# Kernel optimization log

Measured on AMD Instinct MI355X. Metric: run time of the kernel, lower is better.

## Reference

```python
import jax, jax.numpy as jnp
import numpy as np

B, T, C = 4, 4096, 1024
NEG_INF = -1e38


def setup_inputs() -> dict:
    key = jax.random.key(0)
    ks = jax.random.split(key, 5)
    scale = 0.02  # realistic init scale for CxC projections
    x = jax.random.normal(ks[0], (B, T, C), dtype=jnp.float32)
    key_w = jax.random.normal(ks[1], (C, C), dtype=jnp.float32) * scale
    value_w = jax.random.normal(ks[2], (C, C), dtype=jnp.float32) * scale
    receptance_w = jax.random.normal(ks[3], (C, C), dtype=jnp.float32) * scale
    output_w = jax.random.normal(ks[4], (C, C), dtype=jnp.float32) * scale
    # deterministic param init matching the module's __init__
    time_decay = -5.0 + 8.0 * (jnp.arange(C, dtype=jnp.float32) / (C - 1)) ** 0.7
    time_first = jnp.full((C,), -3.0, dtype=jnp.float32)
    # initial WKV state as in forward() when state is None
    aa0 = jnp.zeros((B, C), dtype=jnp.float32)
    bb0 = jnp.zeros((B, C), dtype=jnp.float32)
    pp0 = jnp.full((B, C), NEG_INF, dtype=jnp.float32)
    return dict(x=x, key_w=key_w, value_w=value_w, receptance_w=receptance_w,
                output_w=output_w, time_decay=time_decay, time_first=time_first,
                aa0=aa0, bb0=bb0, pp0=pp0)


def reference(x, key_w, value_w, receptance_w, output_w,
              time_decay, time_first, aa0, bb0, pp0):
    # projections (torch Linear: y = x @ W.T)
    k = jnp.einsum('btc,dc->btd', x, key_w)        # [B,T,C]
    v = jnp.einsum('btc,dc->btd', x, value_w)      # [B,T,C]
    r = jax.nn.sigmoid(jnp.einsum('btc,dc->btd', x, receptance_w))
    w = jnp.exp(time_decay)  # [C]
    u = time_first           # [C]

    def step(carry, kv):
        aa, bb, pp = carry           # each [B,C]
        kt, vt = kv                  # each [B,C]
        # output at this step (numerically stabilized exp weighting)
        ww = u + kt
        p = jnp.maximum(pp, ww)
        e1 = jnp.exp(pp - p)
        e2 = jnp.exp(ww - p)
        wkv = (e1 * aa + e2 * vt) / (e1 * bb + e2)
        # state update
        ww2 = pp - w
        p2 = jnp.maximum(ww2, kt)
        e1b = jnp.exp(ww2 - p2)
        e2b = jnp.exp(kt - p2)
        return (e1b * aa + e2b * vt, e1b * bb + e2b, p2), wkv

    k_t = jnp.swapaxes(k, 0, 1)  # [T,B,C]
    v_t = jnp.swapaxes(v, 0, 1)
    (aa, bb, pp), wkv = jax.lax.scan(step, (aa0, bb0, pp0), (k_t, v_t))
    wkv = jnp.swapaxes(wkv, 0, 1)  # [B,T,C]

    out = jnp.einsum('btc,dc->btd', r * wkv, output_w)
    return out, aa, bb, pp
```

## Files before the change

kernel.cpp:

```cpp
#include <hip/hip_runtime.h>
#include <stdint.h>

#define BDIM 4
#define TDIM 4096
#define CDIM 1024
#define MDIM (BDIM * TDIM)
#define SSEG 64
#define LSEG 64
#define NCH  (BDIM * CDIM)

#define GK   1024
#define GK2  2048
#define NT32 32

typedef __attribute__((ext_vector_type(8))) short bf16x8;
typedef __attribute__((ext_vector_type(4))) float f32x4;

__device__ __forceinline__ unsigned short f2bf(float f) {
    unsigned u = __builtin_bit_cast(unsigned, f);
    u = u + 0x7fffu + ((u >> 16) & 1u);
    return (unsigned short)(u >> 16);
}
__device__ __forceinline__ float bf2f(unsigned short h) {
    unsigned u = ((unsigned)h) << 16;
    return __builtin_bit_cast(float, u);
}

typedef __attribute__((address_space(1))) const unsigned int g_u32;
typedef __attribute__((address_space(3))) unsigned int l_u32;
__device__ __forceinline__ void gload_lds16(const void* g, void* l) {
    __builtin_amdgcn_global_load_lds((g_u32*)g, (l_u32*)l, 16, 0, 0);
}

__global__ void castall(const float* __restrict__ x,
                        const float* __restrict__ kw, const float* __restrict__ vw,
                        const float* __restrict__ rw, const float* __restrict__ ow,
                        unsigned short* __restrict__ xb,
                        unsigned short* __restrict__ wf, unsigned short* __restrict__ owb) {
    int i = blockIdx.x * 256 + threadIdx.x;
    const float* s;
    unsigned short* d;
    int j;
    if (i < 4194304) {
        s = x; d = xb; j = i;
    } else {
        int k = i - 4194304;
        int m = k >> 18; j = k & 262143;
        s = (m == 0) ? kw : (m == 1) ? vw : (m == 2) ? rw : ow;
        d = (m < 3) ? (wf + (size_t)m * 1048576) : owb;
    }
    float4 f = ((const float4*)s)[j];
    ushort4 o;
    o.x = f2bf(f.x); o.y = f2bf(f.y); o.z = f2bf(f.z); o.w = f2bf(f.w);
    ((ushort4*)d)[j] = o;
}


#define MFMA16(ACCROW, AREG, BREG)                                          \
    _Pragma("unroll") for (int a_ = 0; a_ < 4; ++a_)                        \
    _Pragma("unroll") for (int b_ = 0; b_ < 4; ++b_)                        \
        acc[ACCROW + a_][b_] = __builtin_amdgcn_mfma_f32_16x16x32_bf16(     \
            AREG[a_], BREG[b_], acc[ACCROW + a_][b_], 0, 0, 0);

#define KT32(T, BU, BN)                                                     \
  {                                                                         \
    const int slot  = (T) & 3;                                              \
    const int slotN = ((T) + 1) & 3;                                        \
                          \
    {                                                                       \
        const char* ab = shA + slot * 16384 + wm * 8192 + aoffc;            \
        _Pragma("unroll") for (int m_ = 0; m_ < 4; ++m_)                    \
            a47[m_] = *(const bf16x8*)(ab + (4 + m_) * 1024);               \
    }                                                                       \
    stage((T) + 3, 0);                                                      \
    __builtin_amdgcn_s_barrier();                                           \
    __builtin_amdgcn_s_setprio(1);                                          \
    MFMA16(0, a03, BU)                                                      \
    __builtin_amdgcn_s_setprio(0);                                          \
    if ((T) <= 28)      asm volatile("s_waitcnt vmcnt(6)" ::: "memory");    \
    else if ((T) == 29) asm volatile("s_waitcnt vmcnt(4)" ::: "memory");    \
    else if ((T) == 30) asm volatile("s_waitcnt vmcnt(0)" ::: "memory");    \
    __builtin_amdgcn_s_barrier();                                           \
                \
    if ((T) + 1 < NT32) {                                                   \
        const char* abN = shA + slotN * 16384 + wm * 8192 + aoffc;          \
        const char* bbN = shB + slotN * 16384 + wn * 4096 + aoffc;          \
        _Pragma("unroll") for (int m_ = 0; m_ < 4; ++m_)                    \
            a03[m_] = *(const bf16x8*)(abN + m_ * 1024);                    \
        _Pragma("unroll") for (int n_ = 0; n_ < 4; ++n_)                    \
            BN[n_] = *(const bf16x8*)(bbN + n_ * 1024);                     \
    }                                                                       \
    stage((T) + 3, 1);                                                      \
    __builtin_amdgcn_s_barrier();                                           \
    __builtin_amdgcn_s_setprio(1);                                          \
    MFMA16(4, a47, BU)                                                      \
    __builtin_amdgcn_s_setprio(0);                                          \
    __builtin_amdgcn_s_barrier();                                           \
  }

template <int MODE, int NT>
__global__ __launch_bounds__(512, 2) void gemm256(
    const unsigned short* __restrict__ A,
    const unsigned short* __restrict__ Bw,
    unsigned short* __restrict__ oK, unsigned short* __restrict__ oV,
    unsigned short* __restrict__ oR, float* __restrict__ oF)
{
    extern __shared__ char sh[];
    char* shA = sh;
    char* shB = sh + 65536;

    const int tid  = threadIdx.x;
    const int wave = tid >> 6;
    const int lane = tid & 63;
    const int wm   = wave >> 2;
    const int wn   = wave & 3;
    const int lrow = lane & 15;
    const int koct = lane >> 4;

    const int aoffc = (lrow >> 1) * 128 +
                      ((((lrow & 1) * 64) + koct * 16) ^ (((lrow >> 1) & 7) << 4));

    const int inl  = ((tid & 7) * 16) ^ (((tid >> 3) & 7) << 4);
    const int sg0r = 2 * (tid >> 3) + (inl >> 6);
    const int sgc  = inl & 63;
    const int sd0  = tid * 16;
    const int sd1  = 8192 + tid * 16;

    const int bid = blockIdx.x;
    const int xcd = bid & 7;
    const int idx = bid >> 3;
    const int mt  = xcd * 8 + idx / NT;
    const int nt  = idx % NT;
    const size_t row0 = (size_t)mt * 256;
    const size_t col0 = (size_t)nt * 256;

    const char* gA = (const char*)A  + row0 * GK2;
    const char* gB = (const char*)Bw + col0 * GK2;

    auto stage = [&](int tt, int isB) {
        if (tt >= NT32) return;
        int slot = tt & 3;
        const char* gbase = (isB ? gB : gA) + tt * 64;
        char* lbase = (isB ? shB : shA) + slot * 16384;
        gload_lds16(gbase + (size_t)sg0r * GK2 + sgc, lbase + sd0);
        gload_lds16(gbase + (size_t)(sg0r + 128) * GK2 + sgc, lbase + sd1);
    };

    stage(0, 0); stage(0, 1);
    stage(1, 0); stage(1, 1);
    stage(2, 0); stage(2, 1);
    asm volatile("s_waitcnt vmcnt(8)" ::: "memory");
    __builtin_amdgcn_s_barrier();

    f32x4 acc[8][4] = {};
    bf16x8 a03[4], a47[4], bA[4], bB[4];

    {
        const char* ab0 = shA + wm * 8192 + aoffc;
        const char* bb0 = shB + wn * 4096 + aoffc;
#pragma unroll
        for (int m = 0; m < 4; ++m) a03[m] = *(const bf16x8*)(ab0 + m * 1024);
#pragma unroll
        for (int n = 0; n < 4; ++n) bA[n] = *(const bf16x8*)(bb0 + n * 1024);
    }

    for (int tt = 0; tt < NT32; tt += 2) {
        KT32(tt,     bA, bB)
        KT32(tt + 1, bB, bA)
    }

    const int crow = (lane >> 4) * 4;
    const int ccol = lane & 15;
    if (MODE == 1) {
#pragma unroll
        for (int mi = 0; mi < 8; ++mi)
#pragma unroll
            for (int ni = 0; ni < 4; ++ni) {
                size_t gr = row0 + wm * 128 + mi * 16 + crow;
                size_t gc = col0 + wn * 64 + ni * 16 + ccol;
#pragma unroll
                for (int j = 0; j < 4; ++j)
                    oF[(gr + j) * 1024 + gc] = acc[mi][ni][j];
            }
    } else {
        const int region = nt >> 2;
        unsigned short* dst = (region == 0) ? oK : ((region == 1) ? oV : oR);
        const size_t cb0 = (size_t)(nt & 3) * 256;
#pragma unroll
        for (int mi = 0; mi < 8; ++mi)
#pragma unroll
            for (int ni = 0; ni < 4; ++ni) {
                size_t gr = row0 + wm * 128 + mi * 16 + crow;
                size_t gc = cb0 + wn * 64 + ni * 16 + ccol;
#pragma unroll
                for (int j = 0; j < 4; ++j) {
                    float val = acc[mi][ni][j];
                    if (region == 2) val = 1.0f / (1.0f + __expf(-val));
                    dst[(gr + j) * 1024 + gc] = f2bf(val);
                }
            }
    }
}

__global__ __launch_bounds__(256) void wkv_phase1(
    const unsigned short* __restrict__ kf, const unsigned short* __restrict__ vf,
    const float* __restrict__ td,
    float* __restrict__ segA, float* __restrict__ segB, float* __restrict__ segP)
{
    const int tid  = blockIdx.x * 256 + threadIdx.x;
    const int lane = tid & 63;
    const int wg   = tid >> 6;
    const int cg   = wg & 63;
    const int s    = wg >> 6;
    const int q    = cg * 64 + lane;
    const int b    = q >> 10;
    const int c    = q & (CDIM - 1);

    const float w = __expf(td[c]);

    float aa = 0.0f, bb = 0.0f, pp = -1e38f;
    size_t idx = (size_t)b * TDIM * CDIM + (size_t)(s * LSEG) * CDIM + c;
#pragma unroll 4
    for (int i = 0; i < LSEG; ++i, idx += CDIM) {
        float kt = bf2f(kf[idx]);
        float vt = bf2f(vf[idx]);
        float ww2 = pp - w;
        float p2  = fmaxf(ww2, kt);
        float e1  = __expf(ww2 - p2);
        float e2  = __expf(kt - p2);
        aa = e1 * aa + e2 * vt;
        bb = e1 * bb + e2;
        pp = p2;
    }
    segA[s * NCH + q] = aa;
    segB[s * NCH + q] = bb;
    segP[s * NCH + q] = pp;
}

__global__ __launch_bounds__(256) void wkv_phase2(
    const float* __restrict__ segA, const float* __restrict__ segB, const float* __restrict__ segP,
    const float* __restrict__ td,
    const float* __restrict__ aa0, const float* __restrict__ bb0, const float* __restrict__ pp0,
    float* __restrict__ preA, float* __restrict__ preB, float* __restrict__ preP,
    float* __restrict__ stout)
{
    const int tid = blockIdx.x * 256 + threadIdx.x;
    const int c = tid & (CDIM - 1);
    const float w  = __expf(td[c]);
    const float Lw = (float)LSEG * w;

    float aa = aa0[tid], bb = bb0[tid], pp = pp0[tid];
    for (int s = 0; s < SSEG; ++s) {
        preA[s * NCH + tid] = aa;
        preB[s * NCH + tid] = bb;
        preP[s * NCH + tid] = pp;
        float al = segA[s * NCH + tid];
        float bl = segB[s * NCH + tid];
        float pl = segP[s * NCH + tid];
        float ppd = pp - Lw;
        float p  = fmaxf(ppd, pl);
        float e1 = __expf(ppd - p);
        float e2 = __expf(pl - p);
        aa = e1 * aa + e2 * al;
        bb = e1 * bb + e2 * bl;
        pp = p;
    }
    stout[tid]           = aa;
    stout[NCH + tid]     = bb;
    stout[2 * NCH + tid] = pp;
}

__global__ __launch_bounds__(256) void wkv_phase3(
    const unsigned short* __restrict__ kf, const unsigned short* __restrict__ vf,
    const unsigned short* __restrict__ rb,
    const float* __restrict__ td, const float* __restrict__ tf,
    const float* __restrict__ preA, const float* __restrict__ preB, const float* __restrict__ preP,
    unsigned short* __restrict__ rwkvb)
{
    const int tid  = blockIdx.x * 256 + threadIdx.x;
    const int lane = tid & 63;
    const int wg   = tid >> 6;
    const int cg   = wg & 63;
    const int s    = wg >> 6;
    const int q    = cg * 64 + lane;
    const int b    = q >> 10;
    const int c    = q & (CDIM - 1);

    const float w = __expf(td[c]);
    const float u = tf[c];

    float aa = preA[s * NCH + q];
    float bb = preB[s * NCH + q];
    float pp = preP[s * NCH + q];

    size_t idx = (size_t)b * TDIM * CDIM + (size_t)(s * LSEG) * CDIM + c;
#pragma unroll 4
    for (int i = 0; i < LSEG; ++i, idx += CDIM) {
        float kt = bf2f(kf[idx]);
        float vt = bf2f(vf[idx]);
        float rt = bf2f(rb[idx]);
        float ww = u + kt;
        float p  = fmaxf(pp, ww);
        float e1 = __expf(pp - p);
        float e2 = __expf(ww - p);
        float wkv = (e1 * aa + e2 * vt) / (e1 * bb + e2);
        rwkvb[idx] = f2bf(rt * wkv);
        float ww2 = pp - w;
        float p2  = fmaxf(ww2, kt);
        float e1b = __expf(ww2 - p2);
        float e2b = __expf(kt - p2);
        aa = e1b * aa + e2b * vt;
        bb = e1b * bb + e2b;
        pp = p2;
    }
}

extern "C" void kernel_launch(void* const* d_in, const int* in_sizes, int n_in,
                              void* d_out, int out_size, void* d_ws, size_t ws_size,
                              hipStream_t stream) {
    const float* x   = (const float*)d_in[0];
    const float* kw  = (const float*)d_in[1];
    const float* vw  = (const float*)d_in[2];
    const float* rw  = (const float*)d_in[3];
    const float* ow  = (const float*)d_in[4];
    const float* td  = (const float*)d_in[5];
    const float* tf  = (const float*)d_in[6];
    const float* aa0 = (const float*)d_in[7];
    const float* bb0 = (const float*)d_in[8];
    const float* pp0 = (const float*)d_in[9];
    float* out = (float*)d_out;

    char* ws = (char*)d_ws;
    unsigned short* wf    = (unsigned short*)(ws);
    unsigned short* owb   = (unsigned short*)(ws + 6291456);
    unsigned short* xb    = (unsigned short*)(ws + 8388608);
    unsigned short* kfb   = (unsigned short*)(ws + 41943040);
    unsigned short* vfb   = (unsigned short*)(ws + 75497472);
    unsigned short* rbb   = (unsigned short*)(ws + 109051904);
    unsigned short* rwkvb = (unsigned short*)(ws + 142606336);
    float* segA = (float*)(ws + 176160768);
    float* segB = (float*)(ws + 177209344);
    float* segP = (float*)(ws + 178257920);
    float* preA = (float*)(ws + 179306496);
    float* preB = (float*)(ws + 180355072);
    float* preP = (float*)(ws + 181403648);

    hipFuncSetAttribute((const void*)(gemm256<0, 12>), hipFuncAttributeMaxDynamicSharedMemorySize, 131072);
    hipFuncSetAttribute((const void*)(gemm256<1, 4>),  hipFuncAttributeMaxDynamicSharedMemorySize, 131072);

    castall<<<20480, 256, 0, stream>>>(x, kw, vw, rw, ow, xb, wf, owb);

    gemm256<0, 12><<<768, 512, 131072, stream>>>(xb, wf, kfb, vfb, rbb, nullptr);

    wkv_phase1<<<NCH * SSEG / 256, 256, 0, stream>>>(kfb, vfb, td, segA, segB, segP);
    wkv_phase2<<<NCH / 256, 256, 0, stream>>>(segA, segB, segP, td, aa0, bb0, pp0,
                                              preA, preB, preP, out + (size_t)MDIM * CDIM);
    wkv_phase3<<<NCH * SSEG / 256, 256, 0, stream>>>(kfb, vfb, rbb, td, tf,
                                                     preA, preB, preP, rwkvb);

    gemm256<1, 4><<<256, 512, 131072, stream>>>(rwkvb, owb, nullptr, nullptr, nullptr, out);
}
```

Baseline: 226.3 us.

## Replace 256x256 multi-stage GEMM with simpler 128x128 double-buffered GEMM

```diff
diff --git a/kernel.cpp b/kernel.cpp
--- a/kernel.cpp
+++ b/kernel.cpp
@@ -9,9 +9,8 @@
 #define LSEG 64
 #define NCH  (BDIM * CDIM)
 
-#define GK   1024
 #define GK2  2048
-#define NT32 32
+#define NK32 32
 
 typedef __attribute__((ext_vector_type(8))) short bf16x8;
 typedef __attribute__((ext_vector_type(4))) float f32x4;
@@ -55,142 +54,103 @@
     ((ushort4*)d)[j] = o;
 }
 
-
-#define MFMA16(ACCROW, AREG, BREG)                                          \
-    _Pragma("unroll") for (int a_ = 0; a_ < 4; ++a_)                        \
-    _Pragma("unroll") for (int b_ = 0; b_ < 4; ++b_)                        \
-        acc[ACCROW + a_][b_] = __builtin_amdgcn_mfma_f32_16x16x32_bf16(     \
-            AREG[a_], BREG[b_], acc[ACCROW + a_][b_], 0, 0, 0);
-
-#define KT32(T, BU, BN)                                                     \
-  {                                                                         \
-    const int slot  = (T) & 3;                                              \
-    const int slotN = ((T) + 1) & 3;                                        \
-                          \
-    {                                                                       \
-        const char* ab = shA + slot * 16384 + wm * 8192 + aoffc;            \
-        _Pragma("unroll") for (int m_ = 0; m_ < 4; ++m_)                    \
-            a47[m_] = *(const bf16x8*)(ab + (4 + m_) * 1024);               \
-    }                                                                       \
-    stage((T) + 3, 0);                                                      \
-    __builtin_amdgcn_s_barrier();                                           \
-    __builtin_amdgcn_s_setprio(1);                                          \
-    MFMA16(0, a03, BU)                                                      \
-    __builtin_amdgcn_s_setprio(0);                                          \
-    if ((T) <= 28)      asm volatile("s_waitcnt vmcnt(6)" ::: "memory");    \
-    else if ((T) == 29) asm volatile("s_waitcnt vmcnt(4)" ::: "memory");    \
-    else if ((T) == 30) asm volatile("s_waitcnt vmcnt(0)" ::: "memory");    \
-    __builtin_amdgcn_s_barrier();                                           \
-                \
-    if ((T) + 1 < NT32) {                                                   \
-        const char* abN = shA + slotN * 16384 + wm * 8192 + aoffc;          \
-        const char* bbN = shB + slotN * 16384 + wn * 4096 + aoffc;          \
-        _Pragma("unroll") for (int m_ = 0; m_ < 4; ++m_)                    \
-            a03[m_] = *(const bf16x8*)(abN + m_ * 1024);                    \
-        _Pragma("unroll") for (int n_ = 0; n_ < 4; ++n_)                    \
-            BN[n_] = *(const bf16x8*)(bbN + n_ * 1024);                     \
-    }                                                                       \
-    stage((T) + 3, 1);                                                      \
-    __builtin_amdgcn_s_barrier();                                           \
-    __builtin_amdgcn_s_setprio(1);                                          \
-    MFMA16(4, a47, BU)                                                      \
-    __builtin_amdgcn_s_setprio(0);                                          \
-    __builtin_amdgcn_s_barrier();                                           \
-  }
-
 template <int MODE, int NT>
-__global__ __launch_bounds__(512, 2) void gemm256(
+__global__ __launch_bounds__(256, 4) void gemm128(
     const unsigned short* __restrict__ A,
     const unsigned short* __restrict__ Bw,
     unsigned short* __restrict__ oK, unsigned short* __restrict__ oV,
     unsigned short* __restrict__ oR, float* __restrict__ oF)
 {
-    extern __shared__ char sh[];
-    char* shA = sh;
-    char* shB = sh + 65536;
+    __shared__ char sh[32768];
 
     const int tid  = threadIdx.x;
     const int wave = tid >> 6;
     const int lane = tid & 63;
-    const int wm   = wave >> 2;
-    const int wn   = wave & 3;
+    const int wm   = wave >> 1;
+    const int wn   = wave & 1;
     const int lrow = lane & 15;
     const int koct = lane >> 4;
 
-    const int aoffc = (lrow >> 1) * 128 +
-                      ((((lrow & 1) * 64) + koct * 16) ^ (((lrow >> 1) & 7) << 4));
-
-    const int inl  = ((tid & 7) * 16) ^ (((tid >> 3) & 7) << 4);
-    const int sg0r = 2 * (tid >> 3) + (inl >> 6);
-    const int sgc  = inl & 63;
-    const int sd0  = tid * 16;
-    const int sd1  = 8192 + tid * 16;
+    const int ao = (wm * 64 + lrow) * 64 + koct * 16;
+    const int bo = (wn * 64 + lrow) * 64 + koct * 16;
+
+    const int r0  = tid >> 2;
+    const int c0  = (tid & 3) * 16;
+    const int s0  = r0 * GK2 + c0;
+    const int s1  = (r0 + 64) * GK2 + c0;
+    const int d0  = tid * 16;
+    const int d1  = 4096 + tid * 16;
 
     const int bid = blockIdx.x;
     const int xcd = bid & 7;
     const int idx = bid >> 3;
-    const int mt  = xcd * 8 + idx / NT;
+    const int mt  = xcd * 16 + idx / NT;
     const int nt  = idx % NT;
-    const size_t row0 = (size_t)mt * 256;
-    const size_t col0 = (size_t)nt * 256;
+    const size_t row0 = (size_t)mt * 128;
+    const size_t col0 = (size_t)nt * 128;
 
     const char* gA = (const char*)A  + row0 * GK2;
     const char* gB = (const char*)Bw + col0 * GK2;
 
-    auto stage = [&](int tt, int isB) {
-        if (tt >= NT32) return;
-        int slot = tt & 3;
-        const char* gbase = (isB ? gB : gA) + tt * 64;
-        char* lbase = (isB ? shB : shA) + slot * 16384;
-        gload_lds16(gbase + (size_t)sg0r * GK2 + sgc, lbase + sd0);
-        gload_lds16(gbase + (size_t)(sg0r + 128) * GK2 + sgc, lbase + sd1);
+    auto stage = [&](int tt) {
+        if (tt >= NK32) return;
+        char* lb = sh + (tt & 1) * 8192;
+        const char* ga = gA + tt * 64;
+        const char* gb = gB + tt * 64;
+        gload_lds16(ga + s0, lb + d0);
+        gload_lds16(ga + s1, lb + d1);
+        gload_lds16(gb + s0, lb + 16384 + d0);
+        gload_lds16(gb + s1, lb + 16384 + d1);
     };
 
-    stage(0, 0); stage(0, 1);
-    stage(1, 0); stage(1, 1);
-    stage(2, 0); stage(2, 1);
-    asm volatile("s_waitcnt vmcnt(8)" ::: "memory");
+    stage(0);
+    asm volatile("s_waitcnt vmcnt(0)" ::: "memory");
     __builtin_amdgcn_s_barrier();
 
-    f32x4 acc[8][4] = {};
-    bf16x8 a03[4], a47[4], bA[4], bB[4];
-
-    {
-        const char* ab0 = shA + wm * 8192 + aoffc;
-        const char* bb0 = shB + wn * 4096 + aoffc;
-#pragma unroll
-        for (int m = 0; m < 4; ++m) a03[m] = *(const bf16x8*)(ab0 + m * 1024);
-#pragma unroll
-        for (int n = 0; n < 4; ++n) bA[n] = *(const bf16x8*)(bb0 + n * 1024);
-    }
-
-    for (int tt = 0; tt < NT32; tt += 2) {
-        KT32(tt,     bA, bB)
-        KT32(tt + 1, bB, bA)
+    f32x4 acc[4][4] = {};
+    bf16x8 af[4], bf_[4];
+
+    for (int t = 0; t < NK32; ++t) {
+        stage(t + 1);
+        const char* ab = sh + (t & 1) * 8192 + ao;
+        const char* bb = sh + (t & 1) * 8192 + 16384 + bo;
+#pragma unroll
+        for (int mi = 0; mi < 4; ++mi) af[mi]  = *(const bf16x8*)(ab + mi * 1024);
+#pragma unroll
+        for (int ni = 0; ni < 4; ++ni) bf_[ni] = *(const bf16x8*)(bb + ni * 1024);
+        __builtin_amdgcn_s_setprio(1);
+#pragma unroll
+        for (int mi = 0; mi < 4; ++mi)
+#pragma unroll
+            for (int ni = 0; ni < 4; ++ni)
+                acc[mi][ni] = __builtin_amdgcn_mfma_f32_16x16x32_bf16(af[mi], bf_[ni], acc[mi][ni], 0, 0, 0);
+        __builtin_amdgcn_s_setprio(0);
+        asm volatile("s_waitcnt vmcnt(0)" ::: "memory");
+        __builtin_amdgcn_s_barrier();
     }
 
     const int crow = (lane >> 4) * 4;
     const int ccol = lane & 15;
     if (MODE == 1) {
 #pragma unroll
-        for (int mi = 0; mi < 8; ++mi)
+        for (int mi = 0; mi < 4; ++mi)
 #pragma unroll
             for (int ni = 0; ni < 4; ++ni) {
-                size_t gr = row0 + wm * 128 + mi * 16 + crow;
+                size_t gr = row0 + wm * 64 + mi * 16 + crow;
                 size_t gc = col0 + wn * 64 + ni * 16 + ccol;
 #pragma unroll
                 for (int j = 0; j < 4; ++j)
                     oF[(gr + j) * 1024 + gc] = acc[mi][ni][j];
             }
     } else {
-        const int region = nt >> 2;
+        const int region = nt >> 3;
         unsigned short* dst = (region == 0) ? oK : ((region == 1) ? oV : oR);
-        const size_t cb0 = (size_t)(nt & 3) * 256;
-#pragma unroll
-        for (int mi = 0; mi < 8; ++mi)
+        const size_t cb0 = (size_t)(nt & 7) * 128;
+#pragma unroll
+        for (int mi = 0; mi < 4; ++mi)
 #pragma unroll
             for (int ni = 0; ni < 4; ++ni) {
-                size_t gr = row0 + wm * 128 + mi * 16 + crow;
+                size_t gr = row0 + wm * 64 + mi * 16 + crow;
                 size_t gc = cb0 + wn * 64 + ni * 16 + ccol;
 #pragma unroll
                 for (int j = 0; j < 4; ++j) {
@@ -345,12 +305,9 @@
     float* preB = (float*)(ws + 180355072);
     float* preP = (float*)(ws + 181403648);
 
-    hipFuncSetAttribute((const void*)(gemm256<0, 12>), hipFuncAttributeMaxDynamicSharedMemorySize, 131072);
-    hipFuncSetAttribute((const void*)(gemm256<1, 4>),  hipFuncAttributeMaxDynamicSharedMemorySize, 131072);
-
     castall<<<20480, 256, 0, stream>>>(x, kw, vw, rw, ow, xb, wf, owb);
 
-    gemm256<0, 12><<<768, 512, 131072, stream>>>(xb, wf, kfb, vfb, rbb, nullptr);
+    gemm128<0, 24><<<3072, 256, 0, stream>>>(xb, wf, kfb, vfb, rbb, nullptr);
 
     wkv_phase1<<<NCH * SSEG / 256, 256, 0, stream>>>(kfb, vfb, td, segA, segB, segP);
     wkv_phase2<<<NCH / 256, 256, 0, stream>>>(segA, segB, segP, td, aa0, bb0, pp0,
@@ -358,5 +315,5 @@
     wkv_phase3<<<NCH * SSEG / 256, 256, 0, stream>>>(kfb, vfb, rbb, td, tf,
                                                      preA, preB, preP, rwkvb);
 
-    gemm256<1, 4><<<256, 512, 131072, stream>>>(rwkvb, owb, nullptr, nullptr, nullptr, out);
-}
+    gemm128<1, 8><<<1024, 256, 0, stream>>>(rwkvb, owb, nullptr, nullptr, nullptr, out);
+}
```

New measurement: 247.6 us. 9.4% more time.
